# Performance work log

Measured on AMD Instinct MI355X. Metric: run time of the kernel, lower is better.

The kernel has to match this reference:

```python
import jax, jax.numpy as jnp
import numpy as np

V, D, H, B, T = 32000, 256, 512, 32, 64


def setup_inputs() -> dict:
    key = jax.random.key(0)
    ks = jax.random.split(key, 8)
    return {
        "word_indices": jax.random.randint(ks[0], (B, T), 0, V),
        "num_words": jax.random.randint(ks[1], (B,), 1, T + 1),
        "encoder_state": jax.random.normal(ks[2], (B, H), jnp.float32),
        # learned params
        "embW": jax.random.uniform(ks[3], (V, D), jnp.float32, -1.0, 1.0),
        "Wg": jax.random.normal(ks[4], (D + H, 2 * H), jnp.float32) * 0.05,  # reset+update gates
        "bg": jnp.ones((2 * H,), jnp.float32),  # TF GRUCell gate bias init = 1.0
        "Wc": jax.random.normal(ks[5], (D + H, H), jnp.float32) * 0.05,      # candidate
        "bc": jnp.zeros((H,), jnp.float32),
        "Wout": jax.random.normal(ks[6], (H, V), jnp.float32) * 0.05,        # Dense(V)
        "bout": jnp.zeros((V,), jnp.float32),
    }


def reference(word_indices, num_words, encoder_state, embW, Wg, bg, Wc, bc, Wout, bout):
    # Embedding lookup: [B, T, D] -> time-major [T, B, D]
    xs = jnp.swapaxes(embW[word_indices], 0, 1)
    # sequence-length mask like tf.nn.static_rnn: [T, B, 1]
    mask = (jnp.arange(T)[:, None] < num_words[None, :])[..., None].astype(xs.dtype)

    def step(h, inp):
        x_t, m_t = inp  # [B, D], [B, 1]
        xh = jnp.concatenate([x_t, h], axis=-1)          # [B, D+H]
        r, u = jnp.split(jax.nn.sigmoid(xh @ Wg + bg), 2, axis=-1)
        c = jnp.tanh(jnp.concatenate([x_t, r * h], axis=-1) @ Wc + bc)
        h_new = u * h + (1.0 - u) * c
        out = h_new * m_t                                 # zero outputs past seq length
        h_next = m_t * h_new + (1.0 - m_t) * h            # carry state past seq length
        return h_next, out

    _, outs = jax.lax.scan(step, encoder_state, (xs, mask))  # outs: [T, B, H]
    logits = jnp.einsum('tbh,hv->btv', outs, Wout) + bout    # [B, T, V]
    return logits
```

## Files before the change

### kernel.cpp

```cpp
#include <hip/hip_runtime.h>
#include <hip/hip_bf16.h>

#define V_ 32000
#define D_ 256
#define H_ 512
#define B_ 32
#define T_ 64
#define NSL 8

typedef __attribute__((ext_vector_type(8))) __bf16 bf16x8;
typedef __attribute__((ext_vector_type(4))) float f32x4;
typedef _Float16 f16x2 __attribute__((ext_vector_type(2)));
typedef unsigned int u32t;
typedef unsigned short u16t;
typedef unsigned long long u64t;

__device__ __forceinline__ u32t pack_h16(float a, float b) {
  union { _Float16 h; unsigned short u; } lo, hi;
  lo.h = (_Float16)a; hi.h = (_Float16)b;
  return (u32t)lo.u | ((u32t)hi.u << 16);
}

__device__ __forceinline__ float f16u_to_f(u16t u) {
  union { _Float16 h; unsigned short u; } x;
  x.u = u;
  return (float)x.h;
}

__device__ __forceinline__ float dot2(u32t w, u32t h, float acc) {
#if __has_builtin(__builtin_amdgcn_fdot2)
  return __builtin_amdgcn_fdot2(__builtin_bit_cast(f16x2, w),
                                __builtin_bit_cast(f16x2, h), acc, false);
#else
  f16x2 a = __builtin_bit_cast(f16x2, w);
  f16x2 b = __builtin_bit_cast(f16x2, h);
  return acc + (float)a.x * (float)b.x + (float)a.y * (float)b.y;
#endif
}

__device__ __forceinline__ void gld_lds16(const void* g, void* l) {
  __builtin_amdgcn_global_load_lds((const __attribute__((address_space(1))) void*)g,
                                   (__attribute__((address_space(3))) void*)l,
                                   16, 0, 0);
}

__device__ __forceinline__ u32t ld_rlx(const u32t* p) {
  return __hip_atomic_load(p, __ATOMIC_RELAXED, __HIP_MEMORY_SCOPE_AGENT);
}
__device__ __forceinline__ void st_rlx(u32t* p, u32t v) {
  __hip_atomic_store(p, v, __ATOMIC_RELAXED, __HIP_MEMORY_SCOPE_AGENT);
}

__global__ __launch_bounds__(256) void k_setup(const float* __restrict__ Wout,
                                               __hip_bfloat16* __restrict__ WoutT,
                                               const float* __restrict__ Wg,
                                               const float* __restrict__ Wc,
                                               const float* __restrict__ enc,
                                               uint4* __restrict__ Wg2,
                                               uint4* __restrict__ Wc2,
                                               u32t* __restrict__ HBT,
                                               u32t* __restrict__ RHT,
                                               const int* __restrict__ widx,
                                               const float* __restrict__ embW,
                                               const float* __restrict__ bg,
                                               const float* __restrict__ bc,
                                               float* __restrict__ pre_g,
                                               float* __restrict__ pre_c) {
  int blk = blockIdx.x;
  int tid = threadIdx.x;

  if (blk < 4000) {
    __shared__ float tile[64][65];
    int v0 = (blk % 500) * 64;
    int h0 = (blk / 500) * 64;
#pragma unroll
    for (int i = 0; i < 16; ++i) {
      int idx = i * 256 + tid;
      int r = idx >> 6;
      int c = idx & 63;
      tile[r][c] = Wout[(size_t)(h0 + r) * V_ + v0 + c];
    }
    __syncthreads();
#pragma unroll
    for (int i = 0; i < 16; ++i) {
      int idx = i * 256 + tid;
      int rv = idx >> 6;
      int ch = idx & 63;
      WoutT[(size_t)(v0 + rv) * H_ + h0 + ch] = __float2bfloat16(tile[ch][rv]);
    }
  } else if (blk < 4448) {
    int pblk = blk - 4000;
    if (pblk < 256) {
      int gid = pblk * 256 + tid;
      int ks = gid & 3;
      int cq = (gid >> 2) & 127;
      int it = (gid >> 9) & 15;
      int s = gid >> 13;
      int j = (cq < 64) ? (s * 64 + cq) : (512 + s * 64 + (cq - 64));
      int k0 = ks * 128 + it * 8;
      uint4 v;
      v.x = pack_h16(Wg[(size_t)(256 + k0 + 0) * 1024 + j], Wg[(size_t)(256 + k0 + 1) * 1024 + j]);
      v.y = pack_h16(Wg[(size_t)(256 + k0 + 2) * 1024 + j], Wg[(size_t)(256 + k0 + 3) * 1024 + j]);
      v.z = pack_h16(Wg[(size_t)(256 + k0 + 4) * 1024 + j], Wg[(size_t)(256 + k0 + 5) * 1024 + j]);
      v.w = pack_h16(Wg[(size_t)(256 + k0 + 6) * 1024 + j], Wg[(size_t)(256 + k0 + 7) * 1024 + j]);
      Wg2[gid] = v;
    } else if (pblk < 384) {
      int gid = (pblk - 256) * 256 + tid;
      int ks8 = gid & 7;
      int cq2 = (gid >> 3) & 63;
      int it = (gid >> 9) & 7;
      int s = gid >> 12;
      int jc = s * 64 + cq2;
      int k0 = ks8 * 64 + it * 8;
      uint4 v;
      v.x = pack_h16(Wc[(size_t)(256 + k0 + 0) * 512 + jc], Wc[(size_t)(256 + k0 + 1) * 512 + jc]);
      v.y = pack_h16(Wc[(size_t)(256 + k0 + 2) * 512 + jc], Wc[(size_t)(256 + k0 + 3) * 512 + jc]);
      v.z = pack_h16(Wc[(size_t)(256 + k0 + 4) * 512 + jc], Wc[(size_t)(256 + k0 + 5) * 512 + jc]);
      v.w = pack_h16(Wc[(size_t)(256 + k0 + 6) * 512 + jc], Wc[(size_t)(256 + k0 + 7) * 512 + jc]);
      Wc2[gid] = v;
    } else {
      int gid = (pblk - 384) * 256 + tid;
      int b = gid >> 9, k = gid & 511;
      u32t hv = pack_h16(enc[b * H_ + k], 0.f) & 0xffffu;
      st_rlx(&HBT[gid], hv);
      st_rlx(&RHT[gid], 0xFFFF0000u);
    }
  } else {
    __shared__ __align__(16) float x2[D_][8];
    __shared__ int wid[8];
    int idx = blk - 4448;
    int bx = idx & 255;
    int by = idx >> 8;
    int n0 = bx * 8;
    if (tid < 8) wid[tid] = widx[n0 + tid];
    __syncthreads();
#pragma unroll
    for (int i = 0; i < 8; ++i)
      x2[tid][i] = embW[(size_t)wid[i] * D_ + tid];
    __syncthreads();

    float acc[8];
    if (by < 4) {
      int J = by * 256 + tid;
      float bias = bg[J];
#pragma unroll
      for (int i = 0; i < 8; ++i) acc[i] = bias;
      for (int d = 0; d < D_; ++d) {
        float4 xa = *(const float4*)&x2[d][0];
        float4 xb = *(const float4*)&x2[d][4];
        float w = Wg[(size_t)d * 1024 + J];
        acc[0] = fmaf(xa.x, w, acc[0]); acc[1] = fmaf(xa.y, w, acc[1]);
        acc[2] = fmaf(xa.z, w, acc[2]); acc[3] = fmaf(xa.w, w, acc[3]);
        acc[4] = fmaf(xb.x, w, acc[4]); acc[5] = fmaf(xb.y, w, acc[5]);
        acc[6] = fmaf(xb.z, w, acc[6]); acc[7] = fmaf(xb.w, w, acc[7]);
      }
#pragma unroll
      for (int i = 0; i < 8; ++i)
        pre_g[(size_t)(n0 + i) * 1024 + J] = acc[i];
    } else {
      int Jc = (by - 4) * 256 + tid;
      float bias = bc[Jc];
#pragma unroll
      for (int i = 0; i < 8; ++i) acc[i] = bias;
      for (int d = 0; d < D_; ++d) {
        float4 xa = *(const float4*)&x2[d][0];
        float4 xb = *(const float4*)&x2[d][4];
        float w = Wc[(size_t)d * 512 + Jc];
        acc[0] = fmaf(xa.x, w, acc[0]); acc[1] = fmaf(xa.y, w, acc[1]);
        acc[2] = fmaf(xa.z, w, acc[2]); acc[3] = fmaf(xa.w, w, acc[3]);
        acc[4] = fmaf(xb.x, w, acc[4]); acc[5] = fmaf(xb.y, w, acc[5]);
        acc[6] = fmaf(xb.z, w, acc[6]); acc[7] = fmaf(xb.w, w, acc[7]);
      }
#pragma unroll
      for (int i = 0; i < 8; ++i)
        pre_c[(size_t)(n0 + i) * 512 + Jc] = acc[i];
    }
  }
}

__global__ __launch_bounds__(512, 2) void k_gru7(const int* __restrict__ num_words,
                                                 const uint4* __restrict__ Wg2,
                                                 const uint4* __restrict__ Wc2,
                                                 const float* __restrict__ pre_g,
                                                 const float* __restrict__ pre_c,
                                                 u32t* __restrict__ RHT,
                                                 u32t* __restrict__ HBT,
                                                 u32t* __restrict__ A32) {
  __shared__ __align__(16) u32t h2_l[256];
  __shared__ __align__(16) u32t rh2_l[256];
  __shared__ float u_l[64];
  int bid = blockIdx.x;
  int b = bid & 31;
  int s = bid >> 5;
  int tid = threadIdx.x;
  int nw = num_words[b];

  int cq = tid >> 2, ks = tid & 3;
  int j1 = (cq < 64) ? (s * 64 + cq) : (512 + s * 64 + (cq - 64));
  int cq2 = tid >> 3, ks8 = tid & 7;
  int jc = s * 64 + cq2;

  uint4 wg[16];
#pragma unroll
  for (int i = 0; i < 16; ++i) {
    int ii = (i + ks) & 15;
    wg[i] = Wg2[(((size_t)s * 16 + ii) * 128 + cq) * 4 + ks];
  }
  uint4 wc[8];
#pragma unroll
  for (int i = 0; i < 8; ++i) {
    int ii = (i + ks8) & 7;
    wc[i] = Wc2[(((size_t)s * 8 + ii) * 64 + cq2) * 8 + ks8];
  }

  u32t* HBp = HBT + (size_t)b * 512;
  u32t* RHp = RHT + (size_t)b * 512;
  bool pub1 = (ks == 0) && (cq < 64);
  bool ulane = (ks == 0) && (cq >= 64);
  bool pub2 = (ks8 == 0);
  bool writer2 = pub2 && ((cq2 & 1) == 0);

  for (int t = 0; t < T_; ++t) {
    float pg = pre_g[((size_t)b * T_ + t) * 1024 + j1];
    float pc = pre_c[((size_t)b * T_ + t) * 512 + jc];

    __syncthreads();
    {
      u32t want = (u32t)t << 16;
      u32t v;
      do { v = ld_rlx(&HBp[tid]); } while ((v & 0xffff0000u) != want);
      ((volatile u16t*)h2_l)[tid] = (u16t)v;
    }
    __syncthreads();

    float a0 = 0.f, a1 = 0.f, a2s = 0.f, a3 = 0.f;
    const uint4* h4 = (const uint4*)h2_l;
#pragma unroll
    for (int i = 0; i < 16; ++i) {
      int ii = (i + ks) & 15;
      uint4 hv = h4[ks * 16 + ii];
      a0 = dot2(wg[i].x, hv.x, a0);
      a1 = dot2(wg[i].y, hv.y, a1);
      a2s = dot2(wg[i].z, hv.z, a2s);
      a3 = dot2(wg[i].w, hv.w, a3);
    }
    float a = (a0 + a1) + (a2s + a3);
    a += __shfl_xor(a, 1);
    a += __shfl_xor(a, 2);
    float gate = 1.f / (1.f + __expf(-(a + pg)));
    if (cq < 64) {
      float hh = f16u_to_f(((const u16t*)h2_l)[s * 64 + cq]);
      if (pub1)
        st_rlx(&RHp[s * 64 + cq],
               (pack_h16(gate * hh, 0.f) & 0xffffu) | ((u32t)(t + 1) << 16));
    } else if (ulane) {
      u_l[cq - 64] = gate;
    }

    {
      u32t want = (u32t)(t + 1) << 16;
      u32t v;
      do { v = ld_rlx(&RHp[tid]); } while ((v & 0xffff0000u) != want);
      ((volatile u16t*)rh2_l)[tid] = (u16t)v;
    }
    __syncthreads();

    float c0 = 0.f, c1 = 0.f, c2 = 0.f, c3 = 0.f;
    const uint4* r4 = (const uint4*)rh2_l;
#pragma unroll
    for (int i = 0; i < 8; ++i) {
      int ii = (i + ks8) & 7;
      uint4 rv = r4[ks8 * 8 + ii];
      c0 = dot2(wc[i].x, rv.x, c0);
      c1 = dot2(wc[i].y, rv.y, c1);
      c2 = dot2(wc[i].z, rv.z, c2);
      c3 = dot2(wc[i].w, rv.w, c3);
    }
    float a2 = (c0 + c1) + (c2 + c3);
    a2 += __shfl_xor(a2, 1);
    a2 += __shfl_xor(a2, 2);
    a2 += __shfl_xor(a2, 4);
    float cv = tanhf(a2 + pc);
    float uu = u_l[cq2];
    float hold = f16u_to_f(((const u16t*)h2_l)[jc]);
    float hn = uu * hold + (1.f - uu) * cv;
    bool live = t < nw;
    float hnext = live ? hn : hold;
    if (pub2)
      st_rlx(&HBp[s * 64 + cq2],
             (pack_h16(hnext, 0.f) & 0xffffu) | ((u32t)(t + 1) << 16));
    u32t ma = (u32t)__hip_bfloat16_raw(__float2bfloat16(live ? hn : 0.f)).x;
    u32t oa = (u32t)__shfl_xor((int)ma, 8);
    if (writer2)
      A32[(((size_t)b * T_ + t) * 512 + jc) >> 1] = ma | (oa << 16);
  }
}

__global__ __launch_bounds__(256) void k_proj(const __hip_bfloat16* __restrict__ Ap,
                                              const __hip_bfloat16* __restrict__ BTp,
                                              const float* __restrict__ bout,
                                              float* __restrict__ C) {
  __shared__ char As[128 * 64 * 2];
  __shared__ char Bs[128 * 64 * 2];
  int tid = threadIdx.x;
  int lane = tid & 63;
  int wave = tid >> 6;
  int bid = blockIdx.x;
  int tau = (bid & 7) * 500 + (bid >> 3);
  int m = tau & 15;
  int n = tau >> 4;
  int m0 = m * 128;
  int n0 = n * 128;
  int wm = wave >> 1, wn = wave & 1;
  f32x4 acc[4][4] = {};

  const char* Ab = (const char*)Ap;
  const char* Bb = (const char*)BTp;

  for (int ks = 0; ks < 8; ++ks) {
    int k0 = ks * 64;
    __syncthreads();
#pragma unroll
    for (int inst = 0; inst < 4; ++inst) {
      int o = inst * 4096 + wave * 1024;
      int ol = o + lane * 16;
      int r = ol >> 7;
      int cb = ol & 127;
      gld_lds16(Ab + ((size_t)(m0 + r) * 512 + k0) * 2 + cb, As + o);
      gld_lds16(Bb + ((size_t)(n0 + r) * 512 + k0) * 2 + cb, Bs + o);
    }
    __syncthreads();
#pragma unroll
    for (int kk = 0; kk < 64; kk += 32) {
      bf16x8 af[4], bfr[4];
      int cbyte = kk * 2 + ((lane >> 4) << 4);
#pragma unroll
      for (int mi = 0; mi < 4; ++mi) {
        int row = wm * 64 + mi * 16 + (lane & 15);
        af[mi] = *(const bf16x8*)(As + row * 128 + cbyte);
      }
#pragma unroll
      for (int ni = 0; ni < 4; ++ni) {
        int row = wn * 64 + ni * 16 + (lane & 15);
        bfr[ni] = *(const bf16x8*)(Bs + row * 128 + cbyte);
      }
#pragma unroll
      for (int mi = 0; mi < 4; ++mi)
#pragma unroll
        for (int ni = 0; ni < 4; ++ni)
          acc[mi][ni] = __builtin_amdgcn_mfma_f32_16x16x32_bf16(bfr[ni], af[mi], acc[mi][ni], 0, 0, 0);
    }
  }
#pragma unroll
  for (int ni = 0; ni < 4; ++ni) {
    int colbase = n0 + wn * 64 + ni * 16 + ((lane >> 4) << 2);
    float4 bb = *(const float4*)&bout[colbase];
#pragma unroll
    for (int mi = 0; mi < 4; ++mi) {
      int row = m0 + wm * 64 + mi * 16 + (lane & 15);
      f32x4 v;
      v.x = acc[mi][ni][0] + bb.x;
      v.y = acc[mi][ni][1] + bb.y;
      v.z = acc[mi][ni][2] + bb.z;
      v.w = acc[mi][ni][3] + bb.w;
      __builtin_nontemporal_store(v, (f32x4*)&C[(size_t)row * V_ + colbase]);
    }
  }
}

extern "C" void kernel_launch(void* const* d_in, const int* in_sizes, int n_in,
                              void* d_out, int out_size, void* d_ws, size_t ws_size,
                              hipStream_t stream) {
  const int* widx = (const int*)d_in[0];
  const int* num_words = (const int*)d_in[1];
  const float* enc = (const float*)d_in[2];
  const float* embW = (const float*)d_in[3];
  const float* Wg = (const float*)d_in[4];
  const float* bg = (const float*)d_in[5];
  const float* Wc = (const float*)d_in[6];
  const float* bc = (const float*)d_in[7];
  const float* Wout = (const float*)d_in[8];
  const float* bout = (const float*)d_in[9];
  float* out = (float*)d_out;

  char* ws = (char*)d_ws;
  float* pre_g = (float*)(ws);
  float* pre_c = (float*)(ws + 8388608);
  __hip_bfloat16* A = (__hip_bfloat16*)(ws + 12582912);
  __hip_bfloat16* WoutT = (__hip_bfloat16*)(ws + 14680064);
  uint4* Wg2 = (uint4*)(ws + 47448064);
  uint4* Wc2 = (uint4*)(ws + 48496640);
  u32t* RHT = (u32t*)(ws + 49020928);
  u32t* HBT = (u32t*)(ws + 49086464);

  hipLaunchKernelGGL(k_setup, dim3(5984), dim3(256), 0, stream,
                     Wout, WoutT, Wg, Wc, enc, Wg2, Wc2, HBT, RHT,
                     widx, embW, bg, bc, pre_g, pre_c);
  hipLaunchKernelGGL(k_gru7, dim3(32 * NSL), dim3(512), 0, stream,
                     num_words, Wg2, Wc2, pre_g, pre_c, RHT, HBT, (u32t*)A);
  hipLaunchKernelGGL(k_proj, dim3(4000), dim3(256), 0, stream, A, WoutT, bout, out);
}
```

Before: 378.5 us.

## Compute reset gates redundantly per block to drop the cross-block r·h exchange

```diff
diff --git a/kernel.cpp b/kernel.cpp
--- a/kernel.cpp
+++ b/kernel.cpp
@@ -56,10 +56,10 @@
                                                const float* __restrict__ Wg,
                                                const float* __restrict__ Wc,
                                                const float* __restrict__ enc,
-                                               uint4* __restrict__ Wg2,
+                                               uint4* __restrict__ Wgr,
+                                               uint4* __restrict__ Wu2,
                                                uint4* __restrict__ Wc2,
                                                u32t* __restrict__ HBT,
-                                               u32t* __restrict__ RHT,
                                                const int* __restrict__ widx,
                                                const float* __restrict__ embW,
                                                const float* __restrict__ bg,
@@ -90,20 +90,31 @@
     }
   } else if (blk < 4448) {
     int pblk = blk - 4000;
-    if (pblk < 256) {
+    if (pblk < 128) {
       int gid = pblk * 256 + tid;
-      int ks = gid & 3;
-      int cq = (gid >> 2) & 127;
-      int it = (gid >> 9) & 15;
-      int s = gid >> 13;
-      int j = (cq < 64) ? (s * 64 + cq) : (512 + s * 64 + (cq - 64));
-      int k0 = ks * 128 + it * 8;
+      int i = gid & 63;
+      int j = gid >> 6;
+      int k0 = i * 8;
       uint4 v;
       v.x = pack_h16(Wg[(size_t)(256 + k0 + 0) * 1024 + j], Wg[(size_t)(256 + k0 + 1) * 1024 + j]);
       v.y = pack_h16(Wg[(size_t)(256 + k0 + 2) * 1024 + j], Wg[(size_t)(256 + k0 + 3) * 1024 + j]);
       v.z = pack_h16(Wg[(size_t)(256 + k0 + 4) * 1024 + j], Wg[(size_t)(256 + k0 + 5) * 1024 + j]);
       v.w = pack_h16(Wg[(size_t)(256 + k0 + 6) * 1024 + j], Wg[(size_t)(256 + k0 + 7) * 1024 + j]);
-      Wg2[gid] = v;
+      Wgr[gid] = v;
+    } else if (pblk < 256) {
+      int gid = (pblk - 128) * 256 + tid;
+      int ks8 = gid & 7;
+      int cq2 = (gid >> 3) & 63;
+      int it = (gid >> 9) & 7;
+      int s = gid >> 12;
+      int j = 512 + s * 64 + cq2;
+      int k0 = ks8 * 64 + it * 8;
+      uint4 v;
+      v.x = pack_h16(Wg[(size_t)(256 + k0 + 0) * 1024 + j], Wg[(size_t)(256 + k0 + 1) * 1024 + j]);
+      v.y = pack_h16(Wg[(size_t)(256 + k0 + 2) * 1024 + j], Wg[(size_t)(256 + k0 + 3) * 1024 + j]);
+      v.z = pack_h16(Wg[(size_t)(256 + k0 + 4) * 1024 + j], Wg[(size_t)(256 + k0 + 5) * 1024 + j]);
+      v.w = pack_h16(Wg[(size_t)(256 + k0 + 6) * 1024 + j], Wg[(size_t)(256 + k0 + 7) * 1024 + j]);
+      Wu2[gid] = v;
     } else if (pblk < 384) {
       int gid = (pblk - 256) * 256 + tid;
       int ks8 = gid & 7;
@@ -123,7 +134,6 @@
       int b = gid >> 9, k = gid & 511;
       u32t hv = pack_h16(enc[b * H_ + k], 0.f) & 0xffffu;
       st_rlx(&HBT[gid], hv);
-      st_rlx(&RHT[gid], 0xFFFF0000u);
     }
   } else {
     __shared__ __align__(16) float x2[D_][8];
@@ -178,50 +188,43 @@
   }
 }
 
-__global__ __launch_bounds__(512, 2) void k_gru7(const int* __restrict__ num_words,
-                                                 const uint4* __restrict__ Wg2,
+__global__ __launch_bounds__(512, 1) void k_gru8(const int* __restrict__ num_words,
+                                                 const uint4* __restrict__ Wgr,
+                                                 const uint4* __restrict__ Wu2,
                                                  const uint4* __restrict__ Wc2,
                                                  const float* __restrict__ pre_g,
                                                  const float* __restrict__ pre_c,
-                                                 u32t* __restrict__ RHT,
                                                  u32t* __restrict__ HBT,
                                                  u32t* __restrict__ A32) {
   __shared__ __align__(16) u32t h2_l[256];
   __shared__ __align__(16) u32t rh2_l[256];
-  __shared__ float u_l[64];
   int bid = blockIdx.x;
   int b = bid & 31;
   int s = bid >> 5;
   int tid = threadIdx.x;
   int nw = num_words[b];
 
-  int cq = tid >> 2, ks = tid & 3;
-  int j1 = (cq < 64) ? (s * 64 + cq) : (512 + s * 64 + (cq - 64));
   int cq2 = tid >> 3, ks8 = tid & 7;
   int jc = s * 64 + cq2;
 
-  uint4 wg[16];
-#pragma unroll
-  for (int i = 0; i < 16; ++i) {
-    int ii = (i + ks) & 15;
-    wg[i] = Wg2[(((size_t)s * 16 + ii) * 128 + cq) * 4 + ks];
-  }
-  uint4 wc[8];
+  uint4 wgr[64];
+#pragma unroll
+  for (int i = 0; i < 64; ++i) wgr[i] = Wgr[(size_t)tid * 64 + i];
+  uint4 wu[8], wc[8];
 #pragma unroll
   for (int i = 0; i < 8; ++i) {
     int ii = (i + ks8) & 7;
+    wu[i] = Wu2[(((size_t)s * 8 + ii) * 64 + cq2) * 8 + ks8];
     wc[i] = Wc2[(((size_t)s * 8 + ii) * 64 + cq2) * 8 + ks8];
   }
 
   u32t* HBp = HBT + (size_t)b * 512;
-  u32t* RHp = RHT + (size_t)b * 512;
-  bool pub1 = (ks == 0) && (cq < 64);
-  bool ulane = (ks == 0) && (cq >= 64);
   bool pub2 = (ks8 == 0);
   bool writer2 = pub2 && ((cq2 & 1) == 0);
 
   for (int t = 0; t < T_; ++t) {
-    float pg = pre_g[((size_t)b * T_ + t) * 1024 + j1];
+    float pgr = pre_g[((size_t)b * T_ + t) * 1024 + tid];
+    float pgu = pre_g[((size_t)b * T_ + t) * 1024 + 512 + jc];
     float pc = pre_c[((size_t)b * T_ + t) * 512 + jc];
 
     __syncthreads();
@@ -236,52 +239,45 @@
     float a0 = 0.f, a1 = 0.f, a2s = 0.f, a3 = 0.f;
     const uint4* h4 = (const uint4*)h2_l;
 #pragma unroll
-    for (int i = 0; i < 16; ++i) {
-      int ii = (i + ks) & 15;
-      uint4 hv = h4[ks * 16 + ii];
-      a0 = dot2(wg[i].x, hv.x, a0);
-      a1 = dot2(wg[i].y, hv.y, a1);
-      a2s = dot2(wg[i].z, hv.z, a2s);
-      a3 = dot2(wg[i].w, hv.w, a3);
-    }
-    float a = (a0 + a1) + (a2s + a3);
-    a += __shfl_xor(a, 1);
-    a += __shfl_xor(a, 2);
-    float gate = 1.f / (1.f + __expf(-(a + pg)));
-    if (cq < 64) {
-      float hh = f16u_to_f(((const u16t*)h2_l)[s * 64 + cq]);
-      if (pub1)
-        st_rlx(&RHp[s * 64 + cq],
-               (pack_h16(gate * hh, 0.f) & 0xffffu) | ((u32t)(t + 1) << 16));
-    } else if (ulane) {
-      u_l[cq - 64] = gate;
-    }
-
-    {
-      u32t want = (u32t)(t + 1) << 16;
-      u32t v;
-      do { v = ld_rlx(&RHp[tid]); } while ((v & 0xffff0000u) != want);
-      ((volatile u16t*)rh2_l)[tid] = (u16t)v;
-    }
+    for (int i = 0; i < 64; ++i) {
+      uint4 hv = h4[i];
+      a0 = dot2(wgr[i].x, hv.x, a0);
+      a1 = dot2(wgr[i].y, hv.y, a1);
+      a2s = dot2(wgr[i].z, hv.z, a2s);
+      a3 = dot2(wgr[i].w, hv.w, a3);
+    }
+    float r = 1.f / (1.f + __expf(-((a0 + a1) + (a2s + a3) + pgr)));
+    float hme = f16u_to_f(((const u16t*)h2_l)[tid]);
+    ((volatile u16t*)rh2_l)[tid] = (u16t)(pack_h16(r * hme, 0.f) & 0xffffu);
     __syncthreads();
 
     float c0 = 0.f, c1 = 0.f, c2 = 0.f, c3 = 0.f;
+    float d0 = 0.f, d1 = 0.f, d2 = 0.f, d3 = 0.f;
     const uint4* r4 = (const uint4*)rh2_l;
 #pragma unroll
     for (int i = 0; i < 8; ++i) {
       int ii = (i + ks8) & 7;
       uint4 rv = r4[ks8 * 8 + ii];
+      uint4 hv = h4[ks8 * 8 + ii];
       c0 = dot2(wc[i].x, rv.x, c0);
       c1 = dot2(wc[i].y, rv.y, c1);
       c2 = dot2(wc[i].z, rv.z, c2);
       c3 = dot2(wc[i].w, rv.w, c3);
+      d0 = dot2(wu[i].x, hv.x, d0);
+      d1 = dot2(wu[i].y, hv.y, d1);
+      d2 = dot2(wu[i].z, hv.z, d2);
+      d3 = dot2(wu[i].w, hv.w, d3);
     }
     float a2 = (c0 + c1) + (c2 + c3);
+    float au = (d0 + d1) + (d2 + d3);
     a2 += __shfl_xor(a2, 1);
     a2 += __shfl_xor(a2, 2);
     a2 += __shfl_xor(a2, 4);
+    au += __shfl_xor(au, 1);
+    au += __shfl_xor(au, 2);
+    au += __shfl_xor(au, 4);
     float cv = tanhf(a2 + pc);
-    float uu = u_l[cq2];
+    float uu = 1.f / (1.f + __expf(-(au + pgu)));
     float hold = f16u_to_f(((const u16t*)h2_l)[jc]);
     float hn = uu * hold + (1.f - uu) * cv;
     bool live = t < nw;
@@ -388,15 +384,15 @@
   float* pre_c = (float*)(ws + 8388608);
   __hip_bfloat16* A = (__hip_bfloat16*)(ws + 12582912);
   __hip_bfloat16* WoutT = (__hip_bfloat16*)(ws + 14680064);
-  uint4* Wg2 = (uint4*)(ws + 47448064);
+  uint4* Wgr = (uint4*)(ws + 47448064);
+  uint4* Wu2 = (uint4*)(ws + 47972352);
   uint4* Wc2 = (uint4*)(ws + 48496640);
-  u32t* RHT = (u32t*)(ws + 49020928);
   u32t* HBT = (u32t*)(ws + 49086464);
 
   hipLaunchKernelGGL(k_setup, dim3(5984), dim3(256), 0, stream,
-                     Wout, WoutT, Wg, Wc, enc, Wg2, Wc2, HBT, RHT,
+                     Wout, WoutT, Wg, Wc, enc, Wgr, Wu2, Wc2, HBT,
                      widx, embW, bg, bc, pre_g, pre_c);
-  hipLaunchKernelGGL(k_gru7, dim3(32 * NSL), dim3(512), 0, stream,
-                     num_words, Wg2, Wc2, pre_g, pre_c, RHT, HBT, (u32t*)A);
+  hipLaunchKernelGGL(k_gru8, dim3(32 * NSL), dim3(512), 0, stream,
+                     num_words, Wgr, Wu2, Wc2, pre_g, pre_c, HBT, (u32t*)A);
   hipLaunchKernelGGL(k_proj, dim3(4000), dim3(256), 0, stream, A, WoutT, bout, out);
 }
```

New measurement: 1.192 ms. 215% more time.
